# Kernel optimization log

Hardware: AMD Instinct MI355X
Metric: run time of the kernel (lower is better)

Reference implementation:

```python
import jax, jax.numpy as jnp
import numpy as np

N = 50000        # num_nodes
E = 800000       # num_edges
D_IN = 128
D_OUT = 128
BN_EPS = 1e-5    # torch BatchNorm1d default


def setup_inputs() -> dict:
    key = jax.random.key(0)
    ks = jax.random.split(key, 6)
    x = jax.random.normal(ks[0], (N, D_IN), dtype=jnp.float32)
    edge_index = jax.random.randint(ks[1], (2, E), 0, N, dtype=jnp.int64)
    eps = jnp.zeros((1,), dtype=jnp.float32)  # nn.Parameter(torch.tensor([0.0]))
    lim1 = 1.0 / np.sqrt(D_IN)
    lim2 = 1.0 / np.sqrt(D_OUT)
    W1 = jax.random.uniform(ks[2], (D_OUT, D_IN), jnp.float32, -lim1, lim1)
    b1 = jax.random.uniform(ks[3], (D_OUT,), jnp.float32, -lim1, lim1)
    W2 = jax.random.uniform(ks[4], (D_OUT, D_OUT), jnp.float32, -lim2, lim2)
    b2 = jax.random.uniform(ks[5], (D_OUT,), jnp.float32, -lim2, lim2)
    gamma1 = jnp.ones((D_OUT,), jnp.float32)
    beta1 = jnp.zeros((D_OUT,), jnp.float32)
    gamma2 = jnp.ones((D_OUT,), jnp.float32)
    beta2 = jnp.zeros((D_OUT,), jnp.float32)
    return {"x": x, "edge_index": edge_index, "eps": eps,
            "W1": W1, "b1": b1, "gamma1": gamma1, "beta1": beta1,
            "W2": W2, "b2": b2, "gamma2": gamma2, "beta2": beta2}


def _batch_norm(h, gamma, beta):
    # training-mode BatchNorm1d: biased batch variance, eps=1e-5
    mu = h.mean(axis=0)
    var = h.var(axis=0)
    return gamma * (h - mu) * jax.lax.rsqrt(var + BN_EPS) + beta


def reference(x, edge_index, eps, W1, b1, gamma1, beta1, W2, b2, gamma2, beta2):
    row, col = edge_index[0], edge_index[1]
    # agg[v] = sum_{(v,u) in edges} x[u]   (gather + scatter-add)
    agg = jax.ops.segment_sum(x[col], row, num_segments=N)  # [N, D_IN]
    out = (1.0 + eps) * x + agg                              # [N, D_IN]
    h = jax.nn.relu(_batch_norm(out @ W1.T + b1, gamma1, beta1))
    h = jax.nn.relu(_batch_norm(h @ W2.T + b2, gamma2, beta2))
    return h
```

## Files before the change

### kernel.cpp

```cpp
#include <hip/hip_runtime.h>

#define NN 50000
#define EE 800000
#define DD 128
#define BN_EPS 1e-5f
#define XCONV_B 3125
#define BIN_BLOCKS 200
#define BIN_EDGES 4000
#define NBUCK 1563
#define BCAP 1024
#define NREP 32
#define GEMM_B 782
#define LDA 136

typedef __attribute__((ext_vector_type(8))) short bf16x8;
typedef __attribute__((ext_vector_type(4))) float f32x4;
typedef __attribute__((ext_vector_type(8))) unsigned short u16x8;

__device__ inline unsigned short f2bf(float f) {
  unsigned int u = __float_as_uint(f);
  u = (u + 0x7fffu + ((u >> 16) & 1u)) >> 16;
  return (unsigned short)u;
}
__device__ inline float bf2f(unsigned short b) {
  return __uint_as_float(((unsigned int)b) << 16);
}


__global__ __launch_bounds__(256) void k_prep(const float* __restrict__ x,
                                              const float* __restrict__ W1,
                                              const float* __restrict__ W2,
                                              unsigned short* __restrict__ xb,
                                              unsigned short* __restrict__ W1b,
                                              unsigned short* __restrict__ W2b,
                                              int* __restrict__ bcur,
                                              float* __restrict__ reps) {
  const int b = blockIdx.x;
  const int t = threadIdx.x;
  if (b < XCONV_B) {
    const int gid = b * 256 + t;
    const float4 v0 = ((const float4*)x)[gid * 2];
    const float4 v1 = ((const float4*)x)[gid * 2 + 1];
    ushort4 o0, o1;
    o0.x = f2bf(v0.x); o0.y = f2bf(v0.y); o0.z = f2bf(v0.z); o0.w = f2bf(v0.w);
    o1.x = f2bf(v1.x); o1.y = f2bf(v1.y); o1.z = f2bf(v1.z); o1.w = f2bf(v1.w);
    ((ushort4*)xb)[gid * 2] = o0;
    ((ushort4*)xb)[gid * 2 + 1] = o1;
    if (gid <= NBUCK) bcur[gid] = 0;
    if (gid < 4 * NREP * DD) reps[gid] = 0.0f;
  } else if (b < XCONV_B + 16) {
    const int gid = (b - XCONV_B) * 256 + t;
    const float4 v = ((const float4*)W1)[gid];
    ushort4 o;
    o.x = f2bf(v.x); o.y = f2bf(v.y); o.z = f2bf(v.z); o.w = f2bf(v.w);
    ((ushort4*)W1b)[gid] = o;
  } else {
    const int gid = (b - XCONV_B - 16) * 256 + t;
    const float4 v = ((const float4*)W2)[gid];
    ushort4 o;
    o.x = f2bf(v.x); o.y = f2bf(v.y); o.z = f2bf(v.z); o.w = f2bf(v.w);
    ((ushort4*)W2b)[gid] = o;
  }
}

__global__ __launch_bounds__(256) void k_bin0(const int* __restrict__ rows,
                                              const int* __restrict__ cols,
                                              int* __restrict__ bcur,
                                              unsigned int* __restrict__ bbuf) {
  __shared__ int hist[NBUCK];
  __shared__ int lbase[NBUCK];
  const int t = threadIdx.x;
  for (int i = t; i < NBUCK; i += 256) hist[i] = 0;
  __syncthreads();
  const int e0 = blockIdx.x * BIN_EDGES;
  int er[16], ec[16];
#pragma unroll
  for (int i = 0; i < 16; ++i) {
    const int idx = t + i * 256;
    if (idx < BIN_EDGES) {
      er[i] = rows[e0 + idx];
      ec[i] = cols[e0 + idx];
      atomicAdd(&hist[er[i] >> 5], 1);
    }
  }
  __syncthreads();
  for (int i = t; i < NBUCK; i += 256) {
    const int c = hist[i];
    lbase[i] = (c > 0) ? atomicAdd(&bcur[i], c) : 0;
    hist[i] = 0;
  }
  __syncthreads();
#pragma unroll
  for (int i = 0; i < 16; ++i) {
    const int idx = t + i * 256;
    if (idx < BIN_EDGES) {
      const int bk = er[i] >> 5;
      const int lp = lbase[bk] + atomicAdd(&hist[bk], 1);
      if (lp < BCAP)
        bbuf[(size_t)bk * BCAP + lp] =
            ((unsigned)(er[i] & 31) << 16) | (unsigned)ec[i];
    }
  }
}

__global__ __launch_bounds__(256) void k_aggemm1(
    const unsigned short* __restrict__ xb, const float* __restrict__ eps,
    const int* __restrict__ bcnt, const unsigned int* __restrict__ bbuf,
    const unsigned short* __restrict__ W, const float* __restrict__ bias,
    unsigned short* __restrict__ outb, float* __restrict__ sum1r,
    float* __restrict__ sumsq1r) {
  __shared__ unsigned short scols[BCAP];
  __shared__ unsigned short sA[32 * LDA];
  __shared__ int rcnt[32];
  __shared__ int roff[33];
  __shared__ float bsum[DD];
  __shared__ float bsq[DD];
  const int t = threadIdx.x;
  const int bk = blockIdx.x;
  const int wv = t >> 6;
  const int lane = t & 63;
  const int sub = lane >> 4;
  const int l16 = lane & 15;

  int n = bcnt[bk];
  n = n < BCAP ? n : BCAP;
  if (t < 32) rcnt[t] = 0;
  if (t < DD) { bsum[t] = 0.f; bsq[t] = 0.f; }
  __syncthreads();

  unsigned int ent[4];
  int nl = 0;
  for (int i = t; i < n; i += 256) {
    const unsigned int e = bbuf[(size_t)bk * BCAP + i];
    ent[nl++] = e;
    atomicAdd(&rcnt[e >> 16], 1);
  }
  __syncthreads();
  if (t < 64) {
    int v = (t < 32) ? rcnt[t] : 0;
#pragma unroll
    for (int off = 1; off < 32; off <<= 1) {
      const int u = __shfl_up(v, off);
      if (lane >= off) v += u;
    }
    if (t < 32) roff[t] = v - rcnt[t];
    if (t == 31) roff[32] = v;
    if (t < 32) rcnt[t] = 0;
  }
  __syncthreads();
  for (int i = 0; i < nl; ++i) {
    const int r = ent[i] >> 16;
    const int pos = roff[r] + atomicAdd(&rcnt[r], 1);
    scols[pos] = (unsigned short)(ent[i] & 0xffffu);
  }
  __syncthreads();

  {
    const float s = 1.0f + eps[0];
    for (int r = wv; r < 32; r += 4) {
      const int v = bk * 32 + r;
      float acc[8];
#pragma unroll
      for (int j = 0; j < 8; ++j) acc[j] = 0.f;
      if (v < NN) {
        if (sub == 0) {
          const u16x8 a = *(const u16x8*)(xb + (size_t)v * DD + l16 * 8);
#pragma unroll
          for (int j = 0; j < 8; ++j) acc[j] = s * bf2f(a[j]);
        }
        const int beg = roff[r];
        const int end = roff[r + 1];
        int i = beg + sub;
        for (; i + 12 < end; i += 16) {
          const int u0 = scols[i];
          const int u1 = scols[i + 4];
          const int u2 = scols[i + 8];
          const int u3 = scols[i + 12];
          const u16x8 a = *(const u16x8*)(xb + (size_t)u0 * DD + l16 * 8);
          const u16x8 b = *(const u16x8*)(xb + (size_t)u1 * DD + l16 * 8);
          const u16x8 c = *(const u16x8*)(xb + (size_t)u2 * DD + l16 * 8);
          const u16x8 d = *(const u16x8*)(xb + (size_t)u3 * DD + l16 * 8);
#pragma unroll
          for (int j = 0; j < 8; ++j)
            acc[j] += (bf2f(a[j]) + bf2f(b[j])) + (bf2f(c[j]) + bf2f(d[j]));
        }
        for (; i + 4 < end; i += 8) {
          const int u0 = scols[i];
          const int u1 = scols[i + 4];
          const u16x8 a = *(const u16x8*)(xb + (size_t)u0 * DD + l16 * 8);
          const u16x8 b = *(const u16x8*)(xb + (size_t)u1 * DD + l16 * 8);
#pragma unroll
          for (int j = 0; j < 8; ++j) acc[j] += bf2f(a[j]) + bf2f(b[j]);
        }
        if (i < end) {
          const int u = scols[i];
          const u16x8 a = *(const u16x8*)(xb + (size_t)u * DD + l16 * 8);
#pragma unroll
          for (int j = 0; j < 8; ++j) acc[j] += bf2f(a[j]);
        }
      }
#pragma unroll
      for (int j = 0; j < 8; ++j) {
        acc[j] += __shfl_xor(acc[j], 16);
        acc[j] += __shfl_xor(acc[j], 32);
      }
      if (sub == 0) {
        u16x8 o;
#pragma unroll
        for (int j = 0; j < 8; ++j) o[j] = f2bf(acc[j]);
        *(u16x8*)(&sA[r * LDA + l16 * 8]) = o;
      }
    }
  }
  __syncthreads();

  const int wr = wv & 1;
  const int wc = wv >> 1;
  f32x4 acc[4];
#pragma unroll
  for (int nn = 0; nn < 4; ++nn) acc[nn] = (f32x4){0.f, 0.f, 0.f, 0.f};
#pragma unroll
  for (int kk = 0; kk < 4; ++kk) {
    const bf16x8 af =
        *(const bf16x8*)(&sA[(wr * 16 + l16) * LDA + kk * 32 + sub * 8]);
#pragma unroll
    for (int nn = 0; nn < 4; ++nn) {
      const bf16x8 bf = *(const bf16x8*)(
          W + (size_t)(wc * 64 + nn * 16 + l16) * DD + sub * 8 + kk * 32);
      acc[nn] = __builtin_amdgcn_mfma_f32_16x16x32_bf16(af, bf, acc[nn], 0, 0, 0);
    }
  }
  const int orow0 = bk * 32 + wr * 16 + sub * 4;
#pragma unroll
  for (int nn = 0; nn < 4; ++nn) {
    const int col = wc * 64 + nn * 16 + l16;
    const float bv = bias[col];
    float sv = 0.f, qv = 0.f;
#pragma unroll
    for (int r = 0; r < 4; ++r) {
      const int row = orow0 + r;
      if (row < NN) {
        const float o = acc[nn][r] + bv;
        outb[(size_t)row * DD + col] = f2bf(o);
        sv += o; qv += o * o;
      }
    }
    sv += __shfl_xor(sv, 16); qv += __shfl_xor(qv, 16);
    sv += __shfl_xor(sv, 32); qv += __shfl_xor(qv, 32);
    if (sub == 0) { atomicAdd(&bsum[col], sv); atomicAdd(&bsq[col], qv); }
  }
  __syncthreads();
  if (t < DD) {
    const int rep = (bk & (NREP - 1)) * DD;
    atomicAdd(&sum1r[rep + t], bsum[t]);
    atomicAdd(&sumsq1r[rep + t], bsq[t]);
  }
}

__global__ __launch_bounds__(256) void k_gemm2(const unsigned short* __restrict__ A,
                                               const float* __restrict__ sum1r,
                                               const float* __restrict__ sumsq1r,
                                               const float* __restrict__ gamma,
                                               const float* __restrict__ beta,
                                               const unsigned short* __restrict__ W,
                                               const float* __restrict__ bias,
                                               unsigned short* __restrict__ outb,
                                               float* __restrict__ sum2r,
                                               float* __restrict__ sumsq2r,
                                               const float* __restrict__ gamma2,
                                               const float* __restrict__ beta2,
                                               float* __restrict__ scale2,
                                               float* __restrict__ shift2,
                                               int* __restrict__ done) {
  __shared__ float lsc[DD];
  __shared__ float lsh[DD];
  __shared__ float bsum[DD];
  __shared__ float bsq[DD];
  __shared__ int amlast;
  const int tid = threadIdx.x;
  const int wv = tid >> 6;
  const int lane = tid & 63;
  const int quad = lane >> 4;
  const int l16 = lane & 15;
  if (tid < DD) {
    float sm = 0.f, qm = 0.f;
#pragma unroll
    for (int r = 0; r < NREP; ++r) {
      sm += sum1r[r * DD + tid];
      qm += sumsq1r[r * DD + tid];
    }
    const float inv_n = 1.0f / (float)NN;
    const float mean = sm * inv_n;
    const float var = qm * inv_n - mean * mean;
    const float s = gamma[tid] * rsqrtf(var + BN_EPS);
    lsc[tid] = s;
    lsh[tid] = beta[tid] - mean * s;
    bsum[tid] = 0.f;
    bsq[tid] = 0.f;
  }
  __syncthreads();

  const int rowbase = blockIdx.x * 64 + wv * 16 + l16;
  const int arow = rowbase < NN ? rowbase : NN - 1;
  const unsigned short* aptr = A + (size_t)arow * DD + quad * 8;

  f32x4 acc[8];
#pragma unroll
  for (int n = 0; n < 8; ++n) acc[n] = (f32x4){0.f, 0.f, 0.f, 0.f};
#pragma unroll
  for (int kk = 0; kk < 4; ++kk) {
    const int kbase = kk * 32 + quad * 8;
    const u16x8 a = *(const u16x8*)(aptr + kk * 32);
    const float4 s0 = *(const float4*)&lsc[kbase];
    const float4 s1 = *(const float4*)&lsc[kbase + 4];
    const float4 h0 = *(const float4*)&lsh[kbase];
    const float4 h1 = *(const float4*)&lsh[kbase + 4];
    bf16x8 af;
    af[0] = (short)f2bf(fmaxf(fmaf(s0.x, bf2f(a[0]), h0.x), 0.f));
    af[1] = (short)f2bf(fmaxf(fmaf(s0.y, bf2f(a[1]), h0.y), 0.f));
    af[2] = (short)f2bf(fmaxf(fmaf(s0.z, bf2f(a[2]), h0.z), 0.f));
    af[3] = (short)f2bf(fmaxf(fmaf(s0.w, bf2f(a[3]), h0.w), 0.f));
    af[4] = (short)f2bf(fmaxf(fmaf(s1.x, bf2f(a[4]), h1.x), 0.f));
    af[5] = (short)f2bf(fmaxf(fmaf(s1.y, bf2f(a[5]), h1.y), 0.f));
    af[6] = (short)f2bf(fmaxf(fmaf(s1.z, bf2f(a[6]), h1.z), 0.f));
    af[7] = (short)f2bf(fmaxf(fmaf(s1.w, bf2f(a[7]), h1.w), 0.f));
#pragma unroll
    for (int n = 0; n < 8; ++n) {
      const bf16x8 bf =
          *(const bf16x8*)(W + (size_t)(n * 16 + l16) * DD + kbase);
      acc[n] = __builtin_amdgcn_mfma_f32_16x16x32_bf16(af, bf, acc[n], 0, 0, 0);
    }
  }
  const int orow0 = blockIdx.x * 64 + wv * 16 + quad * 4;
#pragma unroll
  for (int n = 0; n < 8; ++n) {
    const int col = n * 16 + l16;
    const float bv = bias[col];
    float sv = 0.f, qv = 0.f;
#pragma unroll
    for (int r = 0; r < 4; ++r) {
      const int row = orow0 + r;
      if (row < NN) {
        const float o = acc[n][r] + bv;
        outb[(size_t)row * DD + col] = f2bf(o);
        sv += o; qv += o * o;
      }
    }
    sv += __shfl_xor(sv, 16); qv += __shfl_xor(qv, 16);
    sv += __shfl_xor(sv, 32); qv += __shfl_xor(qv, 32);
    if (quad == 0) { atomicAdd(&bsum[col], sv); atomicAdd(&bsq[col], qv); }
  }
  __syncthreads();
  if (tid < DD) {
    const int rep = (blockIdx.x & (NREP - 1)) * DD;
    atomicAdd(&sum2r[rep + tid], bsum[tid]);
    atomicAdd(&sumsq2r[rep + tid], bsq[tid]);
  }

  __syncthreads();
  if (tid == 0) amlast = (atomicAdd(done, 1) == GEMM_B - 1) ? 1 : 0;
  __syncthreads();
  if (amlast) {
    if (tid < DD) {
      float sm = 0.f, qm = 0.f;
#pragma unroll
      for (int r = 0; r < NREP; ++r) {
        sm += __hip_atomic_load(&sum2r[r * DD + tid], __ATOMIC_RELAXED,
                                __HIP_MEMORY_SCOPE_AGENT);
        qm += __hip_atomic_load(&sumsq2r[r * DD + tid], __ATOMIC_RELAXED,
                                __HIP_MEMORY_SCOPE_AGENT);
      }
      const float inv_n = 1.0f / (float)NN;
      const float mean = sm * inv_n;
      const float var = qm * inv_n - mean * mean;
      const float sc = gamma2[tid] * rsqrtf(var + BN_EPS);
      scale2[tid] = sc;
      shift2[tid] = beta2[tid] - mean * sc;
    }
  }
}

__global__ __launch_bounds__(256) void k_bnrelu(const unsigned short* __restrict__ in,
                                                const float* __restrict__ scale,
                                                const float* __restrict__ shift,
                                                float* __restrict__ out) {
  __shared__ float lsc[DD];
  __shared__ float lsh[DD];
  const int t = threadIdx.x;
  if (t < DD) {
    lsc[t] = scale[t];
    lsh[t] = shift[t];
  }
  __syncthreads();
  const int gid = blockIdx.x * 256 + t;
  const int c = (gid & 15) * 8;
  const u16x8 a = ((const u16x8*)in)[gid];
  const float4 sc0 = *(const float4*)&lsc[c];
  const float4 sc1 = *(const float4*)&lsc[c + 4];
  const float4 sh0 = *(const float4*)&lsh[c];
  const float4 sh1 = *(const float4*)&lsh[c + 4];
  float4 o0, o1;
  o0.x = fmaxf(fmaf(sc0.x, bf2f(a[0]), sh0.x), 0.f);
  o0.y = fmaxf(fmaf(sc0.y, bf2f(a[1]), sh0.y), 0.f);
  o0.z = fmaxf(fmaf(sc0.z, bf2f(a[2]), sh0.z), 0.f);
  o0.w = fmaxf(fmaf(sc0.w, bf2f(a[3]), sh0.w), 0.f);
  o1.x = fmaxf(fmaf(sc1.x, bf2f(a[4]), sh1.x), 0.f);
  o1.y = fmaxf(fmaf(sc1.y, bf2f(a[5]), sh1.y), 0.f);
  o1.z = fmaxf(fmaf(sc1.z, bf2f(a[6]), sh1.z), 0.f);
  o1.w = fmaxf(fmaf(sc1.w, bf2f(a[7]), sh1.w), 0.f);
  ((float4*)out)[gid * 2] = o0;
  ((float4*)out)[gid * 2 + 1] = o1;
}

extern "C" void kernel_launch(void* const* d_in, const int* in_sizes, int n_in,
                              void* d_out, int out_size, void* d_ws, size_t ws_size,
                              hipStream_t stream) {
  const float* x = (const float*)d_in[0];
  const int* ei = (const int*)d_in[1];
  const float* eps = (const float*)d_in[2];
  const float* W1 = (const float*)d_in[3];
  const float* b1 = (const float*)d_in[4];
  const float* g1 = (const float*)d_in[5];
  const float* be1 = (const float*)d_in[6];
  const float* W2 = (const float*)d_in[7];
  const float* b2 = (const float*)d_in[8];
  const float* g2 = (const float*)d_in[9];
  const float* be2 = (const float*)d_in[10];
  float* out = (float*)d_out;

  const int* rows = ei;
  const int* cols = ei + EE;

  int* bcur = (int*)d_out;
  unsigned short* xb = (unsigned short*)d_out + 2000000;
  unsigned int* bbuf = (unsigned int*)((char*)d_out + 16800000);
  unsigned short* W1b = (unsigned short*)d_out + 11640000;
  unsigned short* W2b = (unsigned short*)d_out + 11680000;
  float* reps = (float*)d_out + 5875000;
  float* sum1r = reps;
  float* sumsq1r = reps + NREP * DD;
  float* sum2r = reps + 2 * NREP * DD;
  float* sumsq2r = reps + 3 * NREP * DD;
  int* done = bcur + NBUCK;

  unsigned short* h1b = (unsigned short*)d_ws;
  unsigned short* h2b = h1b + (size_t)NN * DD;
  float* stats = (float*)(h1b + (size_t)2 * NN * DD);
  float* scale2 = stats + 0;
  float* shift2 = stats + 128;

  k_prep<<<XCONV_B + 32, 256, 0, stream>>>(x, W1, W2, xb, W1b, W2b, bcur, reps);
  k_bin0<<<BIN_BLOCKS, 256, 0, stream>>>(rows, cols, bcur, bbuf);
  k_aggemm1<<<NBUCK, 256, 0, stream>>>(xb, eps, bcur, bbuf, W1b, b1, h1b,
                                       sum1r, sumsq1r);
  k_gemm2<<<GEMM_B, 256, 0, stream>>>(h1b, sum1r, sumsq1r, g1, be1, W2b, b2,
                                      h2b, sum2r, sumsq2r, g2, be2,
                                      scale2, shift2, done);
  k_bnrelu<<<(NN * DD / 8) / 256, 256, 0, stream>>>(h2b, scale2, shift2, out);
}
```

Baseline: 213.0 us.

## Halve aggregation bucket size and interleave two rows per wave for gather ILP

Buckets now hold 16 rows instead of 32, so the fused aggregate+GEMM1 kernel launches twice as many 128-thread blocks. Each wave gathers neighbours for two rows at once to keep more independent loads in flight. The LDS pre-reduction of the BatchNorm statistics is removed in favour of direct global atomics. This aims to improve latency hiding and load balance in the gather phase, at the cost of roughly twice as many global atomics on the replicated stat buffers and less reuse of W per block in the MFMA stage.

New measurement: 209.2 us. No clear change (-1.8%).

```diff
diff --git a/kernel.cpp b/kernel.cpp
--- a/kernel.cpp
+++ b/kernel.cpp
@@ -7,8 +7,9 @@
 #define XCONV_B 3125
 #define BIN_BLOCKS 200
 #define BIN_EDGES 4000
-#define NBUCK 1563
-#define BCAP 1024
+#define NBUCK 3125
+#define BROWS 16
+#define BCAP 512
 #define NREP 32
 #define GEMM_B 782
 #define LDA 136
@@ -80,7 +81,7 @@
     if (idx < BIN_EDGES) {
       er[i] = rows[e0 + idx];
       ec[i] = cols[e0 + idx];
-      atomicAdd(&hist[er[i] >> 5], 1);
+      atomicAdd(&hist[er[i] >> 4], 1);
     }
   }
   __syncthreads();
@@ -94,27 +95,25 @@
   for (int i = 0; i < 16; ++i) {
     const int idx = t + i * 256;
     if (idx < BIN_EDGES) {
-      const int bk = er[i] >> 5;
+      const int bk = er[i] >> 4;
       const int lp = lbase[bk] + atomicAdd(&hist[bk], 1);
       if (lp < BCAP)
         bbuf[(size_t)bk * BCAP + lp] =
-            ((unsigned)(er[i] & 31) << 16) | (unsigned)ec[i];
-    }
-  }
-}
-
-__global__ __launch_bounds__(256) void k_aggemm1(
+            ((unsigned)(er[i] & 15) << 16) | (unsigned)ec[i];
+    }
+  }
+}
+
+__global__ __launch_bounds__(128) void k_aggemm1(
     const unsigned short* __restrict__ xb, const float* __restrict__ eps,
     const int* __restrict__ bcnt, const unsigned int* __restrict__ bbuf,
     const unsigned short* __restrict__ W, const float* __restrict__ bias,
     unsigned short* __restrict__ outb, float* __restrict__ sum1r,
     float* __restrict__ sumsq1r) {
   __shared__ unsigned short scols[BCAP];
-  __shared__ unsigned short sA[32 * LDA];
-  __shared__ int rcnt[32];
-  __shared__ int roff[33];
-  __shared__ float bsum[DD];
-  __shared__ float bsq[DD];
+  __shared__ unsigned short sA[BROWS * LDA];
+  __shared__ int rcnt[BROWS];
+  __shared__ int roff[BROWS + 1];
   const int t = threadIdx.x;
   const int bk = blockIdx.x;
   const int wv = t >> 6;
@@ -124,28 +123,27 @@
 
   int n = bcnt[bk];
   n = n < BCAP ? n : BCAP;
-  if (t < 32) rcnt[t] = 0;
-  if (t < DD) { bsum[t] = 0.f; bsq[t] = 0.f; }
+  if (t < BROWS) rcnt[t] = 0;
   __syncthreads();
 
   unsigned int ent[4];
   int nl = 0;
-  for (int i = t; i < n; i += 256) {
+  for (int i = t; i < n; i += 128) {
     const unsigned int e = bbuf[(size_t)bk * BCAP + i];
     ent[nl++] = e;
     atomicAdd(&rcnt[e >> 16], 1);
   }
   __syncthreads();
-  if (t < 64) {
-    int v = (t < 32) ? rcnt[t] : 0;
-#pragma unroll
-    for (int off = 1; off < 32; off <<= 1) {
+  if (t < BROWS) {
+    int v = rcnt[t];
+#pragma unroll
+    for (int off = 1; off < BROWS; off <<= 1) {
       const int u = __shfl_up(v, off);
       if (lane >= off) v += u;
     }
-    if (t < 32) roff[t] = v - rcnt[t];
-    if (t == 31) roff[32] = v;
-    if (t < 32) rcnt[t] = 0;
+    roff[t] = v - rcnt[t];
+    if (t == BROWS - 1) roff[BROWS] = v;
+    rcnt[t] = 0;
   }
   __syncthreads();
   for (int i = 0; i < nl; ++i) {
@@ -157,103 +155,152 @@
 
   {
     const float s = 1.0f + eps[0];
-    for (int r = wv; r < 32; r += 4) {
-      const int v = bk * 32 + r;
-      float acc[8];
-#pragma unroll
-      for (int j = 0; j < 8; ++j) acc[j] = 0.f;
-      if (v < NN) {
+#pragma unroll
+    for (int rr = 0; rr < 4; ++rr) {
+      const int r0 = wv + rr * 4;
+      const int r1 = r0 + 2;
+      float a0[8], a1[8];
+#pragma unroll
+      for (int j = 0; j < 8; ++j) { a0[j] = 0.f; a1[j] = 0.f; }
+      if (sub < 2) {
+        const int selfrow = bk * BROWS + (sub == 0 ? r0 : r1);
+        const u16x8 a = *(const u16x8*)(xb + (size_t)selfrow * DD + l16 * 8);
         if (sub == 0) {
-          const u16x8 a = *(const u16x8*)(xb + (size_t)v * DD + l16 * 8);
-#pragma unroll
-          for (int j = 0; j < 8; ++j) acc[j] = s * bf2f(a[j]);
+#pragma unroll
+          for (int j = 0; j < 8; ++j) a0[j] = s * bf2f(a[j]);
+        } else {
+#pragma unroll
+          for (int j = 0; j < 8; ++j) a1[j] = s * bf2f(a[j]);
         }
-        const int beg = roff[r];
-        const int end = roff[r + 1];
-        int i = beg + sub;
-        for (; i + 12 < end; i += 16) {
-          const int u0 = scols[i];
-          const int u1 = scols[i + 4];
-          const int u2 = scols[i + 8];
-          const int u3 = scols[i + 12];
-          const u16x8 a = *(const u16x8*)(xb + (size_t)u0 * DD + l16 * 8);
-          const u16x8 b = *(const u16x8*)(xb + (size_t)u1 * DD + l16 * 8);
-          const u16x8 c = *(const u16x8*)(xb + (size_t)u2 * DD + l16 * 8);
-          const u16x8 d = *(const u16x8*)(xb + (size_t)u3 * DD + l16 * 8);
-#pragma unroll
-          for (int j = 0; j < 8; ++j)
-            acc[j] += (bf2f(a[j]) + bf2f(b[j])) + (bf2f(c[j]) + bf2f(d[j]));
+      }
+      int i0 = roff[r0] + sub;
+      const int E0 = roff[r0 + 1];
+      int i1 = roff[r1] + sub;
+      const int E1 = roff[r1 + 1];
+      while (i0 + 12 < E0 && i1 + 12 < E1) {
+        const int u0 = scols[i0], u1 = scols[i0 + 4];
+        const int u2 = scols[i0 + 8], u3 = scols[i0 + 12];
+        const int v0 = scols[i1], v1 = scols[i1 + 4];
+        const int v2 = scols[i1 + 8], v3 = scols[i1 + 12];
+        const u16x8 pa = *(const u16x8*)(xb + (size_t)u0 * DD + l16 * 8);
+        const u16x8 pb = *(const u16x8*)(xb + (size_t)u1 * DD + l16 * 8);
+        const u16x8 pc = *(const u16x8*)(xb + (size_t)u2 * DD + l16 * 8);
+        const u16x8 pd = *(const u16x8*)(xb + (size_t)u3 * DD + l16 * 8);
+        const u16x8 qa = *(const u16x8*)(xb + (size_t)v0 * DD + l16 * 8);
+        const u16x8 qb = *(const u16x8*)(xb + (size_t)v1 * DD + l16 * 8);
+        const u16x8 qc = *(const u16x8*)(xb + (size_t)v2 * DD + l16 * 8);
+        const u16x8 qd = *(const u16x8*)(xb + (size_t)v3 * DD + l16 * 8);
+#pragma unroll
+        for (int j = 0; j < 8; ++j) {
+          a0[j] += (bf2f(pa[j]) + bf2f(pb[j])) + (bf2f(pc[j]) + bf2f(pd[j]));
+          a1[j] += (bf2f(qa[j]) + bf2f(qb[j])) + (bf2f(qc[j]) + bf2f(qd[j]));
         }
-        for (; i + 4 < end; i += 8) {
-          const int u0 = scols[i];
-          const int u1 = scols[i + 4];
-          const u16x8 a = *(const u16x8*)(xb + (size_t)u0 * DD + l16 * 8);
-          const u16x8 b = *(const u16x8*)(xb + (size_t)u1 * DD + l16 * 8);
-#pragma unroll
-          for (int j = 0; j < 8; ++j) acc[j] += bf2f(a[j]) + bf2f(b[j]);
+        i0 += 16;
+        i1 += 16;
+      }
+      for (; i0 + 12 < E0; i0 += 16) {
+        const int u0 = scols[i0], u1 = scols[i0 + 4];
+        const int u2 = scols[i0 + 8], u3 = scols[i0 + 12];
+        const u16x8 pa = *(const u16x8*)(xb + (size_t)u0 * DD + l16 * 8);
+        const u16x8 pb = *(const u16x8*)(xb + (size_t)u1 * DD + l16 * 8);
+        const u16x8 pc = *(const u16x8*)(xb + (size_t)u2 * DD + l16 * 8);
+        const u16x8 pd = *(const u16x8*)(xb + (size_t)u3 * DD + l16 * 8);
+#pragma unroll
+        for (int j = 0; j < 8; ++j)
+          a0[j] += (bf2f(pa[j]) + bf2f(pb[j])) + (bf2f(pc[j]) + bf2f(pd[j]));
+      }
+      for (; i0 + 4 < E0; i0 += 8) {
+        const int u0 = scols[i0], u1 = scols[i0 + 4];
+        const u16x8 pa = *(const u16x8*)(xb + (size_t)u0 * DD + l16 * 8);
+        const u16x8 pb = *(const u16x8*)(xb + (size_t)u1 * DD + l16 * 8);
+#pragma unroll
+        for (int j = 0; j < 8; ++j) a0[j] += bf2f(pa[j]) + bf2f(pb[j]);
+      }
+      if (i0 < E0) {
+        const int u0 = scols[i0];
+        const u16x8 pa = *(const u16x8*)(xb + (size_t)u0 * DD + l16 * 8);
+#pragma unroll
+        for (int j = 0; j < 8; ++j) a0[j] += bf2f(pa[j]);
+      }
+      for (; i1 + 12 < E1; i1 += 16) {
+        const int v0 = scols[i1], v1 = scols[i1 + 4];
+        const int v2 = scols[i1 + 8], v3 = scols[i1 + 12];
+        const u16x8 qa = *(const u16x8*)(xb + (size_t)v0 * DD + l16 * 8);
+        const u16x8 qb = *(const u16x8*)(xb + (size_t)v1 * DD + l16 * 8);
+        const u16x8 qc = *(const u16x8*)(xb + (size_t)v2 * DD + l16 * 8);
+        const u16x8 qd = *(const u16x8*)(xb + (size_t)v3 * DD + l16 * 8);
+#pragma unroll
+        for (int j = 0; j < 8; ++j)
+          a1[j] += (bf2f(qa[j]) + bf2f(qb[j])) + (bf2f(qc[j]) + bf2f(qd[j]));
+      }
+      for (; i1 + 4 < E1; i1 += 8) {
+        const int v0 = scols[i1], v1 = scols[i1 + 4];
+        const u16x8 qa = *(const u16x8*)(xb + (size_t)v0 * DD + l16 * 8);
+        const u16x8 qb = *(const u16x8*)(xb + (size_t)v1 * DD + l16 * 8);
+#pragma unroll
+        for (int j = 0; j < 8; ++j) a1[j] += bf2f(qa[j]) + bf2f(qb[j]);
+      }
+      if (i1 < E1) {
+        const int v0 = scols[i1];
+        const u16x8 qa = *(const u16x8*)(xb + (size_t)v0 * DD + l16 * 8);
+#pragma unroll
+        for (int j = 0; j < 8; ++j) a1[j] += bf2f(qa[j]);
+      }
+#pragma unroll
+      for (int j = 0; j < 8; ++j) {
+        a0[j] += __shfl_xor(a0[j], 16);
+        a0[j] += __shfl_xor(a0[j], 32);
+        a1[j] += __shfl_xor(a1[j], 16);
+        a1[j] += __shfl_xor(a1[j], 32);
+      }
+      if (sub < 2) {
+        u16x8 o;
+        if (sub == 0) {
+#pragma unroll
+          for (int j = 0; j < 8; ++j) o[j] = f2bf(a0[j]);
+          *(u16x8*)(&sA[r0 * LDA + l16 * 8]) = o;
+        } else {
+#pragma unroll
+          for (int j = 0; j < 8; ++j) o[j] = f2bf(a1[j]);
+          *(u16x8*)(&sA[r1 * LDA + l16 * 8]) = o;
         }
-        if (i < end) {
-          const int u = scols[i];
-          const u16x8 a = *(const u16x8*)(xb + (size_t)u * DD + l16 * 8);
-#pragma unroll
-          for (int j = 0; j < 8; ++j) acc[j] += bf2f(a[j]);
-        }
-      }
-#pragma unroll
-      for (int j = 0; j < 8; ++j) {
-        acc[j] += __shfl_xor(acc[j], 16);
-        acc[j] += __shfl_xor(acc[j], 32);
-      }
-      if (sub == 0) {
-        u16x8 o;
-#pragma unroll
-        for (int j = 0; j < 8; ++j) o[j] = f2bf(acc[j]);
-        *(u16x8*)(&sA[r * LDA + l16 * 8]) = o;
-      }
-    }
-  }
-  __syncthreads();
-
-  const int wr = wv & 1;
-  const int wc = wv >> 1;
+      }
+    }
+  }
+  __syncthreads();
+
   f32x4 acc[4];
 #pragma unroll
   for (int nn = 0; nn < 4; ++nn) acc[nn] = (f32x4){0.f, 0.f, 0.f, 0.f};
 #pragma unroll
   for (int kk = 0; kk < 4; ++kk) {
-    const bf16x8 af =
-        *(const bf16x8*)(&sA[(wr * 16 + l16) * LDA + kk * 32 + sub * 8]);
+    const bf16x8 af = *(const bf16x8*)(&sA[l16 * LDA + kk * 32 + sub * 8]);
 #pragma unroll
     for (int nn = 0; nn < 4; ++nn) {
       const bf16x8 bf = *(const bf16x8*)(
-          W + (size_t)(wc * 64 + nn * 16 + l16) * DD + sub * 8 + kk * 32);
+          W + (size_t)(wv * 64 + nn * 16 + l16) * DD + sub * 8 + kk * 32);
       acc[nn] = __builtin_amdgcn_mfma_f32_16x16x32_bf16(af, bf, acc[nn], 0, 0, 0);
     }
   }
-  const int orow0 = bk * 32 + wr * 16 + sub * 4;
+  const int orow0 = bk * BROWS + sub * 4;
+  const int rep = (bk & (NREP - 1)) * DD;
 #pragma unroll
   for (int nn = 0; nn < 4; ++nn) {
-    const int col = wc * 64 + nn * 16 + l16;
+    const int col = wv * 64 + nn * 16 + l16;
     const float bv = bias[col];
     float sv = 0.f, qv = 0.f;
 #pragma unroll
     for (int r = 0; r < 4; ++r) {
-      const int row = orow0 + r;
-      if (row < NN) {
-        const float o = acc[nn][r] + bv;
-        outb[(size_t)row * DD + col] = f2bf(o);
-        sv += o; qv += o * o;
-      }
+      const float o = acc[nn][r] + bv;
+      outb[(size_t)(orow0 + r) * DD + col] = f2bf(o);
+      sv += o; qv += o * o;
     }
     sv += __shfl_xor(sv, 16); qv += __shfl_xor(qv, 16);
     sv += __shfl_xor(sv, 32); qv += __shfl_xor(qv, 32);
-    if (sub == 0) { atomicAdd(&bsum[col], sv); atomicAdd(&bsq[col], qv); }
-  }
-  __syncthreads();
-  if (t < DD) {
-    const int rep = (bk & (NREP - 1)) * DD;
-    atomicAdd(&sum1r[rep + t], bsum[t]);
-    atomicAdd(&sumsq1r[rep + t], bsq[t]);
+    if (sub == 0) {
+      atomicAdd(&sum1r[rep + col], sv);
+      atomicAdd(&sumsq1r[rep + col], qv);
+    }
   }
 }
 
@@ -451,7 +498,7 @@
 
   k_prep<<<XCONV_B + 32, 256, 0, stream>>>(x, W1, W2, xb, W1b, W2b, bcur, reps);
   k_bin0<<<BIN_BLOCKS, 256, 0, stream>>>(rows, cols, bcur, bbuf);
-  k_aggemm1<<<NBUCK, 256, 0, stream>>>(xb, eps, bcur, bbuf, W1b, b1, h1b,
+  k_aggemm1<<<NBUCK, 128, 0, stream>>>(xb, eps, bcur, bbuf, W1b, b1, h1b,
                                        sum1r, sumsq1r);
   k_gemm2<<<GEMM_B, 256, 0, stream>>>(h1b, sum1r, sumsq1r, g1, be1, W2b, b2,
                                       h2b, sum2r, sumsq2r, g2, be2,
```
